# Optimization experiments

Measured on AMD Instinct MI355X. Metric: run time of the kernel, lower is better.

## Reference

```python
import jax, jax.numpy as jnp
import numpy as np

NS, BS, U, NR, NT, D = 256, 7, 8, 4, 8, 2
ITERS, HID = 3, 200
P, NOISE = 100.0, 1e-7
CIN = 2 * NT * D  # block input width: flattened Z1 and Z2


def setup_inputs() -> dict:
    key = jax.random.key(0)
    ks = jax.random.split(key, 21)
    rn = lambda k, s: jax.random.normal(k, s, dtype=jnp.float32)
    inp = {
        'H_re': rn(ks[0], (NS, BS, BS, U, NR, NT)),
        'H_im': rn(ks[1], (NS, BS, BS, U, NR, NT)),
        'V_re': rn(ks[2], (NS, BS, U, NT, D)),
        'V_im': rn(ks[3], (NS, BS, U, NT, D)),
        'w': jnp.ones((U,), jnp.float32),
        'W1_re': rn(ks[4], (ITERS, HID, CIN)) * 0.05,
        'W1_im': rn(ks[5], (ITERS, HID, CIN)) * 0.05,
        'b1_re': rn(ks[6], (ITERS, HID)) * 0.05,
        'b1_im': rn(ks[7], (ITERS, HID)) * 0.05,
        'W2_re': rn(ks[8], (ITERS, HID, HID)) * 0.05,
        'W2_im': rn(ks[9], (ITERS, HID, HID)) * 0.05,
        'b2_re': rn(ks[10], (ITERS, HID)) * 0.05,
        'b2_im': rn(ks[11], (ITERS, HID)) * 0.05,
        'W3_re': rn(ks[12], (ITERS, HID, HID)) * 0.05,
        'W3_im': rn(ks[13], (ITERS, HID, HID)) * 0.05,
        'b3_re': rn(ks[14], (ITERS, HID)) * 0.05,
        'b3_im': rn(ks[15], (ITERS, HID)) * 0.05,
        'W4_re': rn(ks[16], (ITERS, 1, HID)) * 0.05,
        'W4_im': rn(ks[17], (ITERS, 1, HID)) * 0.05,
        'b4_re': rn(ks[18], (ITERS, 1)) * 0.05,
        'b4_im': rn(ks[19], (ITERS, 1)) * 0.05,
    }
    return inp


def _crelu(x):
    # ComplexReLU: relu on real part, imaginary part passes through
    return jax.nn.relu(x.real) + 1j * x.imag


def _clin(x, W, b):
    # torch Linear with complex weights: x @ W.T + b
    return jnp.einsum('...i,oi->...o', x, W) + b


def _iteration(H, V, w, p):
    n = H.shape[0]
    Z = V
    # HV[n,k,l,i,j] = H[n,k,l,i] @ V[n,k,j]  -> [n,BS,BS,U,U,NR,D]
    HV = jnp.einsum('nklirt,nkjtd->nklijrd', H, V)
    ab = jnp.arange(BS)
    au = jnp.arange(U)
    HV2 = HV[:, ab, ab][:, :, au, au]  # HV[:,k,k,i,i] -> [n,BS,U,NR,D]
    # T[n,k,l,i,j] = HV @ HV^H -> [n,BS,BS,U,U,NR,NR]
    T = jnp.einsum('nklijrd,nklijsd->nklijrs', HV, HV.conj())
    I_r = jnp.eye(NR, dtype=HV.dtype)
    # U[n,l,u] = noise*I + sum_{k,j} T[n,k,l,u,j]
    Usum = NOISE * I_r + T.sum(axis=(1, 4))  # [n,BS,U,NR,NR]
    Y = jnp.linalg.solve(Usum, HV2)
    Td = T[:, ab, ab][:, :, au, au]  # T[:,l,l,u,u]
    F = Usum - Td
    Gamma = jnp.einsum('nlurd,nlure->nlude', HV2.conj(), jnp.linalg.solve(F, HV2))
    IG = jnp.eye(D, dtype=HV.dtype) + Gamma  # [n,BS,U,D,D]
    # A[n,l,m,u] = H[n,l,m,u].mH @ Y[n,m,u] -> [n,BS,BS,U,NT,D]
    A = jnp.einsum('nlmurt,nmurd->nlmutd', H.conj(), Y)
    # L[n,l,u] = sum_m A @ IG[m,u] @ A^H -> [n,BS,U,NT,NT]
    L = jnp.einsum('nlmutd,nmude,nlmuse->nluts', A, IG, A.conj())
    All = A[:, ab, ab]  # A[:,l,l] -> [n,BS,U,NT,D]
    Lam = jnp.einsum('nlutd,nlude->nlute', All, IG)
    wv = w.astype(HV.dtype)[None, None, :, None, None]
    Lam = Lam * wv
    L = L * wv
    Z2 = Lam - jnp.einsum('nluts,nlusd->nlutd', L, Z)
    inp = jnp.concatenate([Z.reshape(n, BS, U, NT * D), Z2.reshape(n, BS, U, NT * D)], -1)
    W1, b1, W2, b2, W3, b3, W4, b4 = p
    h = _crelu(_clin(inp, W1, b1))
    h = _crelu(_clin(h, W2, b2))
    h = _crelu(_clin(h, W3, b3))
    step = _clin(h, W4, b4).real  # [n,BS,U,1]
    Vn = Z + step[..., None] * Z2
    fro = (jnp.abs(Vn) ** 2).sum((-2, -1)).sum(2)  # [n,BS]
    scale = jnp.where(fro > P, jnp.sqrt(P / fro), 1.0)
    return Vn * scale[:, :, None, None, None].astype(Vn.dtype)


def reference(H_re, H_im, V_re, V_im, w, W1_re, W1_im, b1_re, b1_im, W2_re, W2_im, b2_re, b2_im, W3_re, W3_im, b3_re, b3_im, W4_re, W4_im, b4_re, b4_im):
    H = (H_re + 1j * H_im).astype(jnp.complex64)
    V = (V_re + 1j * V_im).astype(jnp.complex64)
    # init_input power normalization per (sample, BS)
    fro0 = (jnp.abs(V) ** 2).sum((-2, -1)).sum(2)
    V = V * jnp.sqrt(P / fro0)[:, :, None, None, None].astype(V.dtype)
    c64 = jnp.complex64
    Ws = [(W1_re + 1j * W1_im).astype(c64), (b1_re + 1j * b1_im).astype(c64),
          (W2_re + 1j * W2_im).astype(c64), (b2_re + 1j * b2_im).astype(c64),
          (W3_re + 1j * W3_im).astype(c64), (b3_re + 1j * b3_im).astype(c64),
          (W4_re + 1j * W4_im).astype(c64), (b4_re + 1j * b4_im).astype(c64)]
    for it in range(ITERS):
        p = tuple(a[it] for a in Ws)
        V = _iteration(H, V, w, p)
    return jnp.stack([V.real, V.imag], axis=-1)
```

## Files before the change

kernel.cpp:

```cpp
#include <hip/hip_runtime.h>
#include <math.h>

#define NS 256
#define BS 7
#define UU 8
#define NR 4
#define NT 8
#define DD 2
#define HID 200
#define CIN 32
#define PP 100.0f
#define NOISEF 1e-7f

typedef _Float16 f16x8 __attribute__((ext_vector_type(8)));
typedef float f32x4 __attribute__((ext_vector_type(4)));

#define AST 424
#define AST0 104
#define NTILES 28
#define B1_KC 3
#define B23_KC 13
#define B1_HALVES (B1_KC*NTILES*64*8)
#define B23_HALVES (B23_KC*NTILES*64*8)
#define BITER_HALVES (B1_HALVES + 2*B23_HALVES)

__device__ void chol_solve(const float2 (*A)[NR], const float2 (*B)[DD], float2 (*X)[DD]) {
  float2 L[NR][NR];
  for (int j = 0; j < NR; ++j) {
    float d = A[j][j].x;
    for (int k = 0; k < j; ++k) d -= L[j][k].x * L[j][k].x + L[j][k].y * L[j][k].y;
    float ld = sqrtf(fmaxf(d, 1e-30f));
    L[j][j] = make_float2(ld, 0.f);
    float inv = 1.f / ld;
    for (int i = j + 1; i < NR; ++i) {
      float sr = A[i][j].x, si = A[i][j].y;
      for (int k = 0; k < j; ++k) {
        float2 a = L[i][k], b = L[j][k];
        sr -= a.x * b.x + a.y * b.y;
        si -= a.y * b.x - a.x * b.y;
      }
      L[i][j] = make_float2(sr * inv, si * inv);
    }
  }
  for (int c = 0; c < DD; ++c) {
    float2 z[NR];
    for (int i = 0; i < NR; ++i) {
      float sr = B[i][c].x, si = B[i][c].y;
      for (int k = 0; k < i; ++k) {
        float2 a = L[i][k], zz = z[k];
        sr -= a.x * zz.x - a.y * zz.y;
        si -= a.x * zz.y + a.y * zz.x;
      }
      float inv = 1.f / L[i][i].x;
      z[i] = make_float2(sr * inv, si * inv);
    }
    for (int i = NR - 1; i >= 0; --i) {
      float sr = z[i].x, si = z[i].y;
      for (int k = i + 1; k < NR; ++k) {
        float2 a = L[k][i], xx = X[k][c];
        sr -= a.x * xx.x + a.y * xx.y;
        si -= a.x * xx.y - a.y * xx.x;
      }
      float inv = 1.f / L[i][i].x;
      X[i][c] = make_float2(sr * inv, si * inv);
    }
  }
}

__global__ void k_norm0(const float* __restrict__ Vre, const float* __restrict__ Vim,
                        float2* __restrict__ Vcur) {
  int nl = blockIdx.x;
  int tid = threadIdx.x;
  size_t base = (size_t)nl * 128;
  float re = Vre[base + tid], im = Vim[base + tid];
  float p = re * re + im * im;
  p += __shfl_down(p, 32); p += __shfl_down(p, 16); p += __shfl_down(p, 8);
  p += __shfl_down(p, 4);  p += __shfl_down(p, 2);  p += __shfl_down(p, 1);
  __shared__ float sred[2];
  if ((tid & 63) == 0) sred[tid >> 6] = p;
  __syncthreads();
  float fro = sred[0] + sred[1];
  float sc = sqrtf(PP / fro);
  Vcur[base + tid] = make_float2(re * sc, im * sc);
}

__global__ __launch_bounds__(512) void k_hv(const float* __restrict__ Hre,
    const float* __restrict__ Him, const float2* __restrict__ Vcur,
    float2* __restrict__ Yb, float2* __restrict__ IGb) {
  int nl = blockIdx.x; int l = nl % BS; int n = nl / BS;
  int tid = threadIdx.x;
  int wave = tid >> 6;
  int lane = tid & 63;
  int k = lane >> 3, j = lane & 7;

  __shared__ float2 Hs[1820];
  __shared__ float2 Vs[952];
  __shared__ float2 GsL[8][10];
  __shared__ float2 TdL[8][10];
  __shared__ float2 HV2L[8][8];

  for (int idx = tid; idx < 1792; idx += 512) {
    int kk = idx >> 8, irt = idx & 255;
    size_t off = ((size_t)(n * BS + kk) * BS + l) * 256 + irt;
    Hs[kk * 260 + irt] = make_float2(Hre[off], Him[off]);
  }
  const float2* Vn = Vcur + (size_t)n * 896;
  for (int idx = tid; idx < 896; idx += 512) {
    int kj = idx >> 4, td = idx & 15;
    Vs[kj * 17 + td] = Vn[idx];
  }
  __syncthreads();

  float2 Gu[10];
  #pragma unroll
  for (int q = 0; q < 10; ++q) Gu[q] = make_float2(0.f, 0.f);
  float2 hv[4][2];
  #pragma unroll
  for (int r = 0; r < 4; ++r)
    #pragma unroll
    for (int d = 0; d < 2; ++d) hv[r][d] = make_float2(0.f, 0.f);

  if (k < 7) {
    float2 v[8][2];
    const float2* vp = &Vs[(k * 8 + j) * 17];
    #pragma unroll
    for (int t = 0; t < 8; ++t) { v[t][0] = vp[2 * t]; v[t][1] = vp[2 * t + 1]; }
    #pragma unroll
    for (int r = 0; r < 4; ++r) {
      const float2* hp = &Hs[k * 260 + wave * 32 + r * 8];
      #pragma unroll
      for (int t = 0; t < 8; ++t) {
        float2 h = hp[t];
        #pragma unroll
        for (int d = 0; d < 2; ++d) {
          hv[r][d].x += h.x * v[t][d].x - h.y * v[t][d].y;
          hv[r][d].y += h.x * v[t][d].y + h.y * v[t][d].x;
        }
      }
    }
    int ui = 0;
    #pragma unroll
    for (int r = 0; r < 4; ++r)
      #pragma unroll
      for (int s = r; s < 4; ++s) {
        float gr = 0.f, gi = 0.f;
        #pragma unroll
        for (int d = 0; d < 2; ++d) {
          float2 a = hv[r][d], c = hv[s][d];
          gr += a.x * c.x + a.y * c.y;
          gi += a.y * c.x - a.x * c.y;
        }
        Gu[ui] = make_float2(gr, gi);
        ++ui;
      }
  }
  if (k == l && j == wave) {
    #pragma unroll
    for (int q = 0; q < 10; ++q) TdL[wave][q] = Gu[q];
    #pragma unroll
    for (int r = 0; r < 4; ++r)
      #pragma unroll
      for (int d = 0; d < 2; ++d)
        HV2L[wave][r * 2 + d] = hv[r][d];
  }
  #pragma unroll
  for (int m = 1; m < 64; m <<= 1) {
    #pragma unroll
    for (int q = 0; q < 10; ++q) {
      Gu[q].x += __shfl_xor(Gu[q].x, m);
      Gu[q].y += __shfl_xor(Gu[q].y, m);
    }
  }
  if (lane == 0) {
    #pragma unroll
    for (int q = 0; q < 10; ++q) GsL[wave][q] = Gu[q];
  }
  __syncthreads();

  if (tid < 16) {
    int i = tid & 7, which = tid >> 3;
    float2 M[NR][NR];
    int ui = 0;
    #pragma unroll
    for (int r = 0; r < 4; ++r)
      #pragma unroll
      for (int s = r; s < 4; ++s) {
        float2 g = GsL[i][ui];
        if (which) { float2 td = TdL[i][ui]; g.x -= td.x; g.y -= td.y; }
        ++ui;
        M[r][s] = g;
        M[s][r] = make_float2(g.x, -g.y);
      }
    #pragma unroll
    for (int r = 0; r < 4; ++r) { M[r][r].x += NOISEF; M[r][r].y = 0.f; }
    float2 Bv[NR][DD], X[NR][DD];
    #pragma unroll
    for (int x = 0; x < 8; ++x) Bv[x >> 1][x & 1] = HV2L[i][x];
    chol_solve(M, Bv, X);
    size_t b = (size_t)nl * 8 + i;
    if (!which) {
      #pragma unroll
      for (int x = 0; x < 8; ++x) Yb[b * 8 + x] = X[x >> 1][x & 1];
    } else {
      #pragma unroll
      for (int d = 0; d < DD; ++d)
        #pragma unroll
        for (int e = 0; e < DD; ++e) {
          float gr = (d == e) ? 1.f : 0.f, gi = 0.f;
          #pragma unroll
          for (int r = 0; r < NR; ++r) {
            float2 a = Bv[r][d], x = X[r][e];
            gr += a.x * x.x + a.y * x.y;
            gi += a.x * x.y - a.y * x.x;
          }
          IGb[b * 4 + d * 2 + e] = make_float2(gr, gi);
        }
    }
  }
}

__global__ __launch_bounds__(256) void k_stage2(const float* __restrict__ Hre,
    const float* __restrict__ Him, const float2* __restrict__ Vcur,
    const float2* __restrict__ Yb, const float2* __restrict__ IGb,
    const float* __restrict__ w, float2* __restrict__ Z2out) {
  int nl = blockIdx.x; int l = nl % BS; int n = nl / BS;
  int tid = threadIdx.x;
  __shared__ float2 SM[3686];
  float2* Hsm  = SM;
  float2* Bsm  = SM;
  float2* Lsm  = SM + 952;
  float2* Ysm  = SM + 1792;
  float2* IGsm = SM + 2247;
  float2* Asm  = SM + 2478;
  float2* Lamm = SM + 3430;
  float2* Zlm  = SM + 3558;

  size_t hbase = ((size_t)n * BS + l) * 1792;
  for (int idx = tid; idx < 1792; idx += 256) {
    int t = idx & 7, r = (idx >> 3) & 3, u = (idx >> 5) & 7, m = idx >> 8;
    Hsm[((u * 4 + r) * 7 + m) * 8 + t] = make_float2(Hre[hbase + idx], Him[hbase + idx]);
  }
  const float2* yp = Yb + (size_t)n * 448;
  for (int idx = tid; idx < 448; idx += 256)
    Ysm[(idx >> 6) * 65 + (idx & 63)] = yp[idx];
  const float2* igp = IGb + (size_t)n * 224;
  if (tid < 224) IGsm[(tid >> 5) * 33 + (tid & 31)] = igp[tid];
  const float2* zp = Vcur + (size_t)nl * 128;
  if (tid < 128) Zlm[tid] = zp[tid];
  __syncthreads();

  for (int idx = tid; idx < 896; idx += 256) {
    int u = idx / 112, rem = idx % 112, m = rem >> 4, t = (rem >> 1) & 7, d = rem & 1;
    float ar = 0.f, ai = 0.f;
    #pragma unroll
    for (int r = 0; r < NR; ++r) {
      float2 h = Hsm[((u * 4 + r) * 7 + m) * 8 + t];
      float2 y = Ysm[m * 65 + u * 8 + r * 2 + d];
      ar += h.x * y.x + h.y * y.y;
      ai += h.x * y.y - h.y * y.x;
    }
    Asm[u * 119 + m * 17 + t * 2 + d] = make_float2(ar, ai);
  }
  __syncthreads();

  for (int idx = tid; idx < 896; idx += 256) {
    int u = idx / 112, rem = idx % 112, m = rem >> 4, t = (rem >> 1) & 7, e = rem & 1;
    float br = 0.f, bi = 0.f;
    #pragma unroll
    for (int d = 0; d < DD; ++d) {
      float2 a = Asm[u * 119 + m * 17 + t * 2 + d];
      float2 g = IGsm[m * 33 + u * 4 + d * 2 + e];
      br += a.x * g.x - a.y * g.y;
      bi += a.x * g.y + a.y * g.x;
    }
    Bsm[u * 119 + m * 17 + t * 2 + e] = make_float2(br, bi);
  }
  __syncthreads();

  for (int idx = tid; idx < 512; idx += 256) {
    int u = idx >> 6, t = (idx >> 3) & 7, s = idx & 7;
    float lr = 0.f, li = 0.f;
    #pragma unroll
    for (int m = 0; m < BS; ++m)
      #pragma unroll
      for (int e = 0; e < DD; ++e) {
        float2 bb = Bsm[u * 119 + m * 17 + t * 2 + e];
        float2 ac = Asm[u * 119 + m * 17 + s * 2 + e];
        lr += bb.x * ac.x + bb.y * ac.y;
        li += bb.y * ac.x - bb.x * ac.y;
      }
    float wu = w[u];
    Lsm[(u * 8 + t) * 8 + s] = make_float2(lr * wu, li * wu);
  }
  if (tid < 128) {
    int u = tid >> 4, t = (tid >> 1) & 7, e = tid & 1;
    float ar = 0.f, ai = 0.f;
    #pragma unroll
    for (int d = 0; d < DD; ++d) {
      float2 a = Asm[u * 119 + l * 17 + t * 2 + d];
      float2 g = IGsm[l * 33 + u * 4 + d * 2 + e];
      ar += a.x * g.x - a.y * g.y;
      ai += a.x * g.y + a.y * g.x;
    }
    float wu = w[u];
    Lamm[u * 16 + t * 2 + e] = make_float2(ar * wu, ai * wu);
  }
  __syncthreads();

  if (tid < 128) {
    int u = tid >> 4, t = (tid >> 1) & 7, d = tid & 1;
    float2 lam = Lamm[u * 16 + t * 2 + d];
    float zr = lam.x, zi = lam.y;
    #pragma unroll
    for (int s = 0; s < NT; ++s) {
      float2 Lts = Lsm[(u * 8 + t) * 8 + s];
      float2 z = Zlm[u * 16 + s * 2 + d];
      zr -= Lts.x * z.x - Lts.y * z.y;
      zi -= Lts.x * z.y + Lts.y * z.x;
    }
    Z2out[(size_t)nl * 128 + u * 16 + t * 2 + d] = make_float2(zr, zi);
  }
}

__global__ __launch_bounds__(256) void k_pack(
    const float* __restrict__ W1re, const float* __restrict__ W1im,
    const float* __restrict__ b1re, const float* __restrict__ b1im,
    const float* __restrict__ W2re, const float* __restrict__ W2im,
    const float* __restrict__ b2re, const float* __restrict__ b2im,
    const float* __restrict__ W3re, const float* __restrict__ W3im,
    const float* __restrict__ b3re, const float* __restrict__ b3im,
    _Float16* __restrict__ Bout) {
  int gid = blockIdx.x * 256 + threadIdx.x;
  int lane = gid & 63;
  int rest = gid >> 6;
  int nt = rest % NTILES;
  int id2 = rest / NTILES;
  if (id2 >= 87) return;
  int iter = id2 / 29, kk = id2 % 29;
  int layer, kc;
  if (kk < 3)       { layer = 0; kc = kk; }
  else if (kk < 16) { layer = 1; kc = kk - 3; }
  else              { layer = 2; kc = kk - 16; }
  const float *Wr, *Wi, *br, *bi;
  if (layer == 0) { Wr = W1re + iter*HID*CIN; Wi = W1im + iter*HID*CIN; br = b1re + iter*HID; bi = b1im + iter*HID; }
  else if (layer == 1) { Wr = W2re + iter*HID*HID; Wi = W2im + iter*HID*HID; br = b2re + iter*HID; bi = b2im + iter*HID; }
  else { Wr = W3re + iter*HID*HID; Wi = W3im + iter*HID*HID; br = b3re + iter*HID; bi = b3im + iter*HID; }
  int c = nt * 16 + (lane & 15);
  int o = c >> 1; int odd = c & 1;
  f16x8 frag;
  #pragma unroll
  for (int j = 0; j < 8; ++j) {
    int k = kc * 32 + (lane >> 4) * 8 + j;
    float v = 0.f;
    if (o < HID) {
      if (layer == 0) {
        if (k < 32)       v = odd ? Wi[o*32 + k] : Wr[o*32 + k];
        else if (k < 64)  { int i = k - 32; v = odd ? Wr[o*32 + i] : -Wi[o*32 + i]; }
        else if (k == 64) v = odd ? bi[o] : br[o];
      } else {
        if (k < 200)       v = odd ? Wi[o*200 + k] : Wr[o*200 + k];
        else if (k == 207) v = odd ? bi[o] : br[o];
        else if (k >= 208 && k < 408) { int i = k - 208; v = odd ? Wr[o*200 + i] : -Wi[o*200 + i]; }
      }
    }
    frag[j] = (_Float16)v;
  }
  size_t off = (size_t)iter * BITER_HALVES
             + (layer == 0 ? 0 : (layer == 1 ? B1_HALVES : (B1_HALVES + B23_HALVES)))
             + ((size_t)(kc * NTILES + nt) * 64 + lane) * 8;
  *(f16x8*)(Bout + off) = frag;
}

template<int ASTRIDE, int KC>
__device__ inline void do_gemm(const _Float16* Ain,
                               const _Float16* __restrict__ Bg,
                               _Float16* Aout, int wr, int wc, int lane) {
  f32x4 acc[2][7];
  #pragma unroll
  for (int rt = 0; rt < 2; ++rt)
    #pragma unroll
    for (int nt = 0; nt < 7; ++nt)
      acc[rt][nt] = (f32x4){0.f, 0.f, 0.f, 0.f};
  const int r0 = (lane & 15) + wr * 32, g = lane >> 4;
  const _Float16* bp0 = Bg + ((size_t)(wc * 7) * 64 + lane) * 8;
  f16x8 b[7];
  #pragma unroll
  for (int nt = 0; nt < 7; ++nt) b[nt] = *(const f16x8*)(bp0 + nt * 512);
  f16x8 a0 = *(const f16x8*)(Ain + r0 * ASTRIDE + 8 * g);
  f16x8 a1 = *(const f16x8*)(Ain + (r0 + 16) * ASTRIDE + 8 * g);
  #pragma unroll
  for (int kc = 0; kc < KC; ++kc) {
    f16x8 a0n, a1n, bn[7];
    if (kc + 1 < KC) {
      const _Float16* bpn = bp0 + (size_t)(kc + 1) * (NTILES * 512);
      #pragma unroll
      for (int nt = 0; nt < 7; ++nt) bn[nt] = *(const f16x8*)(bpn + nt * 512);
      a0n = *(const f16x8*)(Ain + r0 * ASTRIDE + (kc + 1) * 32 + 8 * g);
      a1n = *(const f16x8*)(Ain + (r0 + 16) * ASTRIDE + (kc + 1) * 32 + 8 * g);
    }
    #pragma unroll
    for (int nt = 0; nt < 7; ++nt) {
      acc[0][nt] = __builtin_amdgcn_mfma_f32_16x16x32_f16(a0, b[nt], acc[0][nt], 0, 0, 0);
      acc[1][nt] = __builtin_amdgcn_mfma_f32_16x16x32_f16(a1, b[nt], acc[1][nt], 0, 0, 0);
    }
    if (kc + 1 < KC) {
      a0 = a0n; a1 = a1n;
      #pragma unroll
      for (int nt = 0; nt < 7; ++nt) b[nt] = bn[nt];
    }
  }
  int cbase = wc * 7 * 16 + (lane & 15);
  #pragma unroll
  for (int nt = 0; nt < 7; ++nt) {
    int c = cbase + nt * 16;
    int o = c >> 1;
    bool isre = !(c & 1);
    if (o < HID) {
      _Float16* outp = Aout + (isre ? o : 208 + o);
      #pragma unroll
      for (int rt = 0; rt < 2; ++rt)
        #pragma unroll
        for (int q = 0; q < 4; ++q) {
          float v = acc[rt][nt][q];
          if (isre) v = fmaxf(v, 0.f);
          outp[(size_t)(wr * 32 + rt * 16 + g * 4 + q) * AST] = (_Float16)v;
        }
    }
  }
}

__global__ __launch_bounds__(512, 2) void k_mlp_mfma(
    const float2* __restrict__ Vcur, const float2* __restrict__ Z2,
    const _Float16* __restrict__ Bp,
    const float* __restrict__ W4re, const float* __restrict__ W4im,
    const float* __restrict__ b4re,
    float2* __restrict__ Vout) {
  int b = blockIdx.x;
  int tid = threadIdx.x;
  int wave = tid >> 6, lane = tid & 63;
  int wr = wave >> 2, wc = wave & 3;

  __shared__ _Float16 A0[64 * AST0];
  __shared__ _Float16 Abuf[2][64 * AST];
  __shared__ float2 Zs[64][16];
  __shared__ float2 Z2s[64][16];
  __shared__ float w4s[2][HID];
  __shared__ float stepv[64];
  __shared__ float scs[8];

  for (int idx = tid; idx < 1024; idx += 512) {
    ((float2*)Zs)[idx]  = Vcur[(size_t)b * 1024 + idx];
    ((float2*)Z2s)[idx] = Z2[(size_t)b * 1024 + idx];
  }
  for (int idx = tid; idx < HID; idx += 512) {
    w4s[0][idx] = W4re[idx];
    w4s[1][idx] = W4im[idx];
  }
  __syncthreads();

  for (int idx = tid; idx < 64 * AST0; idx += 512) {
    int m = idx / AST0, c = idx % AST0;
    float v;
    if (c < 64) {
      int f = c & 31;
      float2 z = (f < 16) ? Zs[m][f] : Z2s[m][f - 16];
      v = (c >= 32) ? z.y : z.x;
    } else v = (c == 64) ? 1.f : 0.f;
    A0[m * AST0 + c] = (_Float16)v;
  }
  for (int idx = tid; idx < 2 * 64 * 16; idx += 512) {
    int buf = idx >> 10, rem = idx & 1023, m = rem >> 4, p = rem & 15;
    int c = (p < 8) ? (200 + p) : (400 + p);
    Abuf[buf][m * AST + c] = (p == 7) ? (_Float16)1.f : (_Float16)0.f;
  }
  __syncthreads();

  do_gemm<AST0, B1_KC>(A0, Bp, &Abuf[0][0], wr, wc, lane);
  __syncthreads();
  do_gemm<AST, B23_KC>(&Abuf[0][0], Bp + B1_HALVES, &Abuf[1][0], wr, wc, lane);
  __syncthreads();
  do_gemm<AST, B23_KC>(&Abuf[1][0], Bp + B1_HALVES + B23_HALVES, &Abuf[0][0], wr, wc, lane);
  __syncthreads();

  {
    int m = tid >> 3, q = tid & 7;
    float acc = 0.f;
    for (int o = q; o < HID; o += 8) {
      float hr = (float)Abuf[0][m * AST + o];
      float hi = (float)Abuf[0][m * AST + 208 + o];
      acc += hr * w4s[0][o] - hi * w4s[1][o];
    }
    acc += __shfl_down(acc, 4, 8);
    acc += __shfl_down(acc, 2, 8);
    acc += __shfl_down(acc, 1, 8);
    if (q == 0) stepv[m] = acc + b4re[0];
  }
  __syncthreads();

  for (int idx = tid; idx < 1024; idx += 512) {
    int m = idx >> 4, f = idx & 15;
    float st = stepv[m];
    float2 z = Zs[m][f], z2 = Z2s[m][f];
    Zs[m][f] = make_float2(fmaf(st, z2.x, z.x), fmaf(st, z2.y, z.y));
  }
  __syncthreads();

  {
    const float2* vp = &Zs[wave * 8][0];
    float2 v0 = vp[lane * 2], v1 = vp[lane * 2 + 1];
    float p = v0.x * v0.x + v0.y * v0.y + v1.x * v1.x + v1.y * v1.y;
    p += __shfl_down(p, 32); p += __shfl_down(p, 16); p += __shfl_down(p, 8);
    p += __shfl_down(p, 4);  p += __shfl_down(p, 2);  p += __shfl_down(p, 1);
    if (lane == 0) scs[wave] = (p > PP) ? sqrtf(PP / p) : 1.f;
  }
  __syncthreads();
  for (int idx = tid; idx < 1024; idx += 512) {
    float sc = scs[idx >> 7];
    float2 v = ((float2*)Zs)[idx];
    Vout[(size_t)b * 1024 + idx] = make_float2(v.x * sc, v.y * sc);
  }
}

extern "C" void kernel_launch(void* const* d_in, const int* in_sizes, int n_in,
                              void* d_out, int out_size, void* d_ws, size_t ws_size,
                              hipStream_t stream) {
  const float* Hre  = (const float*)d_in[0];
  const float* Him  = (const float*)d_in[1];
  const float* Vre  = (const float*)d_in[2];
  const float* Vim  = (const float*)d_in[3];
  const float* w    = (const float*)d_in[4];
  const float* W1re = (const float*)d_in[5];
  const float* W1im = (const float*)d_in[6];
  const float* b1re = (const float*)d_in[7];
  const float* b1im = (const float*)d_in[8];
  const float* W2re = (const float*)d_in[9];
  const float* W2im = (const float*)d_in[10];
  const float* b2re = (const float*)d_in[11];
  const float* b2im = (const float*)d_in[12];
  const float* W3re = (const float*)d_in[13];
  const float* W3im = (const float*)d_in[14];
  const float* b3re = (const float*)d_in[15];
  const float* b3im = (const float*)d_in[16];
  const float* W4re = (const float*)d_in[17];
  const float* W4im = (const float*)d_in[18];
  const float* b4re = (const float*)d_in[19];

  const size_t NV = (size_t)NS * BS * UU * NT * DD;
  const size_t NB = (size_t)NS * BS * UU;
  float2* Vcur = (float2*)d_ws;
  float2* Z2b  = Vcur + NV;
  float2* Yb   = Z2b + NV;
  float2* IGb  = Yb + NB * 8;
  _Float16* Bpack = (_Float16*)(IGb + NB * 4);

  k_pack<<<609, 256, 0, stream>>>(W1re, W1im, b1re, b1im, W2re, W2im, b2re, b2im,
                                  W3re, W3im, b3re, b3im, Bpack);
  k_norm0<<<NS * BS, 128, 0, stream>>>(Vre, Vim, Vcur);
  for (int it = 0; it < 3; ++it) {
    k_hv<<<NS * BS, 512, 0, stream>>>(Hre, Him, Vcur, Yb, IGb);
    k_stage2<<<NS * BS, 256, 0, stream>>>(Hre, Him, Vcur, Yb, IGb, w, Z2b);
    float2* vout = (it == 2) ? (float2*)d_out : Vcur;
    k_mlp_mfma<<<NS * BS / 8, 512, 0, stream>>>(Vcur, Z2b,
        Bpack + (size_t)it * BITER_HALVES,
        W4re + it * HID, W4im + it * HID, b4re + it, vout);
  }
}
```

Measured before the change: 258.6 us.

## Move per-block Cholesky solves out of k_hv into a separate parallel kernel

Before, each 512-thread k_hv block ended with a barrier and then only 16 threads ran serial Cholesky solves while the rest of the block sat idle. Now k_hv writes the reduced Gram matrices, diagonal terms and HV2 vectors to global buffers and exits. A new k_solve kernel runs all 28672 solves with one thread each across 112 blocks. The cost is an extra launch per iteration plus a global write and read round trip for the intermediates, which need more workspace.

```diff
diff --git a/kernel.cpp b/kernel.cpp
--- a/kernel.cpp
+++ b/kernel.cpp
@@ -86,7 +86,7 @@
 
 __global__ __launch_bounds__(512) void k_hv(const float* __restrict__ Hre,
     const float* __restrict__ Him, const float2* __restrict__ Vcur,
-    float2* __restrict__ Yb, float2* __restrict__ IGb) {
+    float2* __restrict__ Gsb, float2* __restrict__ Tdb, float2* __restrict__ HV2b) {
   int nl = blockIdx.x; int l = nl % BS; int n = nl / BS;
   int tid = threadIdx.x;
   int wave = tid >> 6;
@@ -95,9 +95,6 @@
 
   __shared__ float2 Hs[1820];
   __shared__ float2 Vs[952];
-  __shared__ float2 GsL[8][10];
-  __shared__ float2 TdL[8][10];
-  __shared__ float2 HV2L[8][8];
 
   for (int idx = tid; idx < 1792; idx += 512) {
     int kk = idx >> 8, irt = idx & 255;
@@ -155,13 +152,12 @@
       }
   }
   if (k == l && j == wave) {
-    #pragma unroll
-    for (int q = 0; q < 10; ++q) TdL[wave][q] = Gu[q];
-    #pragma unroll
-    for (int r = 0; r < 4; ++r)
-      #pragma unroll
-      for (int d = 0; d < 2; ++d)
-        HV2L[wave][r * 2 + d] = hv[r][d];
+    float2* tdp = Tdb + (size_t)(nl * 8 + wave) * 10;
+    #pragma unroll
+    for (int q = 0; q < 10; ++q) tdp[q] = Gu[q];
+    float2* h2p = HV2b + (size_t)(nl * 8 + wave) * 8;
+    #pragma unroll
+    for (int x = 0; x < 8; ++x) h2p[x] = hv[x >> 1][x & 1];
   }
   #pragma unroll
   for (int m = 1; m < 64; m <<= 1) {
@@ -172,50 +168,64 @@
     }
   }
   if (lane == 0) {
-    #pragma unroll
-    for (int q = 0; q < 10; ++q) GsL[wave][q] = Gu[q];
-  }
-  __syncthreads();
-
-  if (tid < 16) {
-    int i = tid & 7, which = tid >> 3;
-    float2 M[NR][NR];
+    float2* gp = Gsb + (size_t)(nl * 8 + wave) * 10;
+    #pragma unroll
+    for (int q = 0; q < 10; ++q) gp[q] = Gu[q];
+  }
+}
+
+__global__ __launch_bounds__(256) void k_solve(const float2* __restrict__ Gsb,
+    const float2* __restrict__ Tdb, const float2* __restrict__ HV2b,
+    float2* __restrict__ Yb, float2* __restrict__ IGb) {
+  int gid = blockIdx.x * 256 + threadIdx.x;
+  int which = (gid >= 14336) ? 1 : 0;
+  int b = gid - which * 14336;
+
+  float2 G[10];
+  const float2* gp = Gsb + (size_t)b * 10;
+  #pragma unroll
+  for (int q = 0; q < 10; ++q) G[q] = gp[q];
+  if (which) {
+    const float2* tp = Tdb + (size_t)b * 10;
+    #pragma unroll
+    for (int q = 0; q < 10; ++q) { float2 t = tp[q]; G[q].x -= t.x; G[q].y -= t.y; }
+  }
+  float2 M[NR][NR];
+  {
     int ui = 0;
     #pragma unroll
     for (int r = 0; r < 4; ++r)
       #pragma unroll
       for (int s = r; s < 4; ++s) {
-        float2 g = GsL[i][ui];
-        if (which) { float2 td = TdL[i][ui]; g.x -= td.x; g.y -= td.y; }
+        M[r][s] = G[ui];
+        M[s][r] = make_float2(G[ui].x, -G[ui].y);
         ++ui;
-        M[r][s] = g;
-        M[s][r] = make_float2(g.x, -g.y);
       }
     #pragma unroll
     for (int r = 0; r < 4; ++r) { M[r][r].x += NOISEF; M[r][r].y = 0.f; }
-    float2 Bv[NR][DD], X[NR][DD];
-    #pragma unroll
-    for (int x = 0; x < 8; ++x) Bv[x >> 1][x & 1] = HV2L[i][x];
-    chol_solve(M, Bv, X);
-    size_t b = (size_t)nl * 8 + i;
-    if (!which) {
-      #pragma unroll
-      for (int x = 0; x < 8; ++x) Yb[b * 8 + x] = X[x >> 1][x & 1];
-    } else {
-      #pragma unroll
-      for (int d = 0; d < DD; ++d)
+  }
+  float2 Bv[NR][DD], X[NR][DD];
+  const float2* hp = HV2b + (size_t)b * 8;
+  #pragma unroll
+  for (int x = 0; x < 8; ++x) Bv[x >> 1][x & 1] = hp[x];
+  chol_solve(M, Bv, X);
+  if (!which) {
+    #pragma unroll
+    for (int x = 0; x < 8; ++x) Yb[(size_t)b * 8 + x] = X[x >> 1][x & 1];
+  } else {
+    #pragma unroll
+    for (int d = 0; d < DD; ++d)
+      #pragma unroll
+      for (int e = 0; e < DD; ++e) {
+        float gr = (d == e) ? 1.f : 0.f, gi = 0.f;
         #pragma unroll
-        for (int e = 0; e < DD; ++e) {
-          float gr = (d == e) ? 1.f : 0.f, gi = 0.f;
-          #pragma unroll
-          for (int r = 0; r < NR; ++r) {
-            float2 a = Bv[r][d], x = X[r][e];
-            gr += a.x * x.x + a.y * x.y;
-            gi += a.x * x.y - a.y * x.x;
-          }
-          IGb[b * 4 + d * 2 + e] = make_float2(gr, gi);
+        for (int r = 0; r < NR; ++r) {
+          float2 a = Bv[r][d], x = X[r][e];
+          gr += a.x * x.x + a.y * x.y;
+          gi += a.x * x.y - a.y * x.x;
         }
-    }
+        IGb[(size_t)b * 4 + d * 2 + e] = make_float2(gr, gi);
+      }
   }
 }
 
@@ -551,13 +561,17 @@
   float2* Z2b  = Vcur + NV;
   float2* Yb   = Z2b + NV;
   float2* IGb  = Yb + NB * 8;
-  _Float16* Bpack = (_Float16*)(IGb + NB * 4);
+  float2* Gsb  = IGb + NB * 4;
+  float2* Tdb  = Gsb + NB * 10;
+  float2* HV2b = Tdb + NB * 10;
+  _Float16* Bpack = (_Float16*)(HV2b + NB * 8);
 
   k_pack<<<609, 256, 0, stream>>>(W1re, W1im, b1re, b1im, W2re, W2im, b2re, b2im,
                                   W3re, W3im, b3re, b3im, Bpack);
   k_norm0<<<NS * BS, 128, 0, stream>>>(Vre, Vim, Vcur);
   for (int it = 0; it < 3; ++it) {
-    k_hv<<<NS * BS, 512, 0, stream>>>(Hre, Him, Vcur, Yb, IGb);
+    k_hv<<<NS * BS, 512, 0, stream>>>(Hre, Him, Vcur, Gsb, Tdb, HV2b);
+    k_solve<<<112, 256, 0, stream>>>(Gsb, Tdb, HV2b, Yb, IGb);
     k_stage2<<<NS * BS, 256, 0, stream>>>(Hre, Him, Vcur, Yb, IGb, w, Z2b);
     float2* vout = (it == 2) ? (float2*)d_out : Vcur;
     k_mlp_mfma<<<NS * BS / 8, 512, 0, stream>>>(Vcur, Z2b,
```

Result: faster. 252.1 us (-2.5%).

## Process all BS columns per sample in one k_hv block with double-buffered H loads

Applied to the files above, without the earlier changes.

The HV/Gram kernel now launches one block per sample instead of one per (sample, l). Each block loops over the 7 l values and prefetches the next H slice into registers while computing the current one in a double-buffered LDS tile. V is loaded once per sample rather than once per l, and global loads use float4. The Cholesky solves are batched at the end across 112 threads. The cost is far fewer blocks (256 on a GPU with many CUs) and a serialized l loop, so parallelism and latency hiding may suffer.

```diff
diff --git a/kernel.cpp b/kernel.cpp
--- a/kernel.cpp
+++ b/kernel.cpp
@@ -84,137 +84,166 @@
   Vcur[base + tid] = make_float2(re * sc, im * sc);
 }
 
-__global__ __launch_bounds__(512) void k_hv(const float* __restrict__ Hre,
+__global__ __launch_bounds__(512, 2) void k_hv_n(const float* __restrict__ Hre,
     const float* __restrict__ Him, const float2* __restrict__ Vcur,
     float2* __restrict__ Yb, float2* __restrict__ IGb) {
-  int nl = blockIdx.x; int l = nl % BS; int n = nl / BS;
+  int n = blockIdx.x;
   int tid = threadIdx.x;
   int wave = tid >> 6;
   int lane = tid & 63;
-  int k = lane >> 3, j = lane & 7;
-
-  __shared__ float2 Hs[1820];
+  int kl = lane >> 3, j = lane & 7;
+
+  __shared__ float2 Hbuf[2][1820];
   __shared__ float2 Vs[952];
-  __shared__ float2 GsL[8][10];
-  __shared__ float2 TdL[8][10];
-  __shared__ float2 HV2L[8][8];
-
-  for (int idx = tid; idx < 1792; idx += 512) {
-    int kk = idx >> 8, irt = idx & 255;
-    size_t off = ((size_t)(n * BS + kk) * BS + l) * 256 + irt;
-    Hs[kk * 260 + irt] = make_float2(Hre[off], Him[off]);
-  }
+  __shared__ float2 GsL[56][10];
+  __shared__ float2 TdL[56][10];
+  __shared__ float2 HV2L[56][8];
+
+  const int kk = tid >> 6;
+  const int irt = (tid & 63) * 4;
+
   const float2* Vn = Vcur + (size_t)n * 896;
-  for (int idx = tid; idx < 896; idx += 512) {
-    int kj = idx >> 4, td = idx & 15;
-    Vs[kj * 17 + td] = Vn[idx];
-  }
-  __syncthreads();
-
-  float2 Gu[10];
-  #pragma unroll
-  for (int q = 0; q < 10; ++q) Gu[q] = make_float2(0.f, 0.f);
-  float2 hv[4][2];
-  #pragma unroll
-  for (int r = 0; r < 4; ++r)
-    #pragma unroll
-    for (int d = 0; d < 2; ++d) hv[r][d] = make_float2(0.f, 0.f);
-
-  if (k < 7) {
-    float2 v[8][2];
-    const float2* vp = &Vs[(k * 8 + j) * 17];
+  if (tid < 448) {
+    size_t off = ((size_t)(n * BS + kk) * BS + 0) * 256 + irt;
+    float4 r0 = *(const float4*)(Hre + off);
+    float4 i0 = *(const float4*)(Him + off);
+    float2* hb = &Hbuf[0][kk * 260 + irt];
+    ((float4*)hb)[0] = make_float4(r0.x, i0.x, r0.y, i0.y);
+    ((float4*)hb)[1] = make_float4(r0.z, i0.z, r0.w, i0.w);
+    int row = tid >> 3, c = (tid & 7) * 2;
+    float4 vv = *(const float4*)((const float*)(Vn + row * 16 + c));
+    Vs[row * 17 + c]     = make_float2(vv.x, vv.y);
+    Vs[row * 17 + c + 1] = make_float2(vv.z, vv.w);
+  }
+  __syncthreads();
+
+  float2 v[8][2];
+  if (kl < 7) {
+    const float2* vp = &Vs[(kl * 8 + j) * 17];
     #pragma unroll
     for (int t = 0; t < 8; ++t) { v[t][0] = vp[2 * t]; v[t][1] = vp[2 * t + 1]; }
-    #pragma unroll
-    for (int r = 0; r < 4; ++r) {
-      const float2* hp = &Hs[k * 260 + wave * 32 + r * 8];
-      #pragma unroll
-      for (int t = 0; t < 8; ++t) {
-        float2 h = hp[t];
+  }
+
+  float4 hreN, himN;
+  #pragma unroll 1
+  for (int l = 0; l < BS; ++l) {
+    if (l + 1 < BS && tid < 448) {
+      size_t off = ((size_t)(n * BS + kk) * BS + (l + 1)) * 256 + irt;
+      hreN = *(const float4*)(Hre + off);
+      himN = *(const float4*)(Him + off);
+    }
+    const float2* Hc = &Hbuf[l & 1][0];
+
+    float2 Gu[10];
+    #pragma unroll
+    for (int q = 0; q < 10; ++q) Gu[q] = make_float2(0.f, 0.f);
+    float2 hv[4][2];
+    #pragma unroll
+    for (int r = 0; r < 4; ++r)
+      #pragma unroll
+      for (int d = 0; d < 2; ++d) hv[r][d] = make_float2(0.f, 0.f);
+
+    if (kl < 7) {
+      #pragma unroll
+      for (int r = 0; r < 4; ++r) {
+        const float2* hp = &Hc[kl * 260 + wave * 32 + r * 8];
         #pragma unroll
-        for (int d = 0; d < 2; ++d) {
-          hv[r][d].x += h.x * v[t][d].x - h.y * v[t][d].y;
-          hv[r][d].y += h.x * v[t][d].y + h.y * v[t][d].x;
+        for (int t = 0; t < 8; ++t) {
+          float2 h = hp[t];
+          #pragma unroll
+          for (int d = 0; d < 2; ++d) {
+            hv[r][d].x += h.x * v[t][d].x - h.y * v[t][d].y;
+            hv[r][d].y += h.x * v[t][d].y + h.y * v[t][d].x;
+          }
         }
       }
-    }
-    int ui = 0;
-    #pragma unroll
-    for (int r = 0; r < 4; ++r)
-      #pragma unroll
-      for (int s = r; s < 4; ++s) {
-        float gr = 0.f, gi = 0.f;
+      int ui = 0;
+      #pragma unroll
+      for (int r = 0; r < 4; ++r)
         #pragma unroll
-        for (int d = 0; d < 2; ++d) {
-          float2 a = hv[r][d], c = hv[s][d];
-          gr += a.x * c.x + a.y * c.y;
-          gi += a.y * c.x - a.x * c.y;
+        for (int s = r; s < 4; ++s) {
+          float gr = 0.f, gi = 0.f;
+          #pragma unroll
+          for (int d = 0; d < 2; ++d) {
+            float2 a = hv[r][d], c = hv[s][d];
+            gr += a.x * c.x + a.y * c.y;
+            gi += a.y * c.x - a.x * c.y;
+          }
+          Gu[ui] = make_float2(gr, gi);
+          ++ui;
         }
-        Gu[ui] = make_float2(gr, gi);
-        ++ui;
-      }
-  }
-  if (k == l && j == wave) {
-    #pragma unroll
-    for (int q = 0; q < 10; ++q) TdL[wave][q] = Gu[q];
-    #pragma unroll
-    for (int r = 0; r < 4; ++r)
-      #pragma unroll
-      for (int d = 0; d < 2; ++d)
-        HV2L[wave][r * 2 + d] = hv[r][d];
-  }
-  #pragma unroll
-  for (int m = 1; m < 64; m <<= 1) {
-    #pragma unroll
-    for (int q = 0; q < 10; ++q) {
-      Gu[q].x += __shfl_xor(Gu[q].x, m);
-      Gu[q].y += __shfl_xor(Gu[q].y, m);
-    }
-  }
-  if (lane == 0) {
-    #pragma unroll
-    for (int q = 0; q < 10; ++q) GsL[wave][q] = Gu[q];
-  }
-  __syncthreads();
-
-  if (tid < 16) {
-    int i = tid & 7, which = tid >> 3;
-    float2 M[NR][NR];
-    int ui = 0;
-    #pragma unroll
-    for (int r = 0; r < 4; ++r)
-      #pragma unroll
-      for (int s = r; s < 4; ++s) {
-        float2 g = GsL[i][ui];
-        if (which) { float2 td = TdL[i][ui]; g.x -= td.x; g.y -= td.y; }
-        ++ui;
-        M[r][s] = g;
-        M[s][r] = make_float2(g.x, -g.y);
-      }
-    #pragma unroll
-    for (int r = 0; r < 4; ++r) { M[r][r].x += NOISEF; M[r][r].y = 0.f; }
-    float2 Bv[NR][DD], X[NR][DD];
-    #pragma unroll
-    for (int x = 0; x < 8; ++x) Bv[x >> 1][x & 1] = HV2L[i][x];
-    chol_solve(M, Bv, X);
-    size_t b = (size_t)nl * 8 + i;
-    if (!which) {
-      #pragma unroll
-      for (int x = 0; x < 8; ++x) Yb[b * 8 + x] = X[x >> 1][x & 1];
-    } else {
-      #pragma unroll
-      for (int d = 0; d < DD; ++d)
+    }
+    if (kl == l && j == wave) {
+      #pragma unroll
+      for (int q = 0; q < 10; ++q) TdL[l * 8 + wave][q] = Gu[q];
+      #pragma unroll
+      for (int x = 0; x < 8; ++x) HV2L[l * 8 + wave][x] = hv[x >> 1][x & 1];
+    }
+    #pragma unroll
+    for (int m = 1; m < 64; m <<= 1) {
+      #pragma unroll
+      for (int q = 0; q < 10; ++q) {
+        Gu[q].x += __shfl_xor(Gu[q].x, m);
+        Gu[q].y += __shfl_xor(Gu[q].y, m);
+      }
+    }
+    if (lane == 0) {
+      #pragma unroll
+      for (int q = 0; q < 10; ++q) GsL[l * 8 + wave][q] = Gu[q];
+    }
+
+    __syncthreads();
+    if (l + 1 < BS) {
+      if (tid < 448) {
+        float2* hb = &Hbuf[(l + 1) & 1][kk * 260 + irt];
+        ((float4*)hb)[0] = make_float4(hreN.x, himN.x, hreN.y, himN.y);
+        ((float4*)hb)[1] = make_float4(hreN.z, himN.z, hreN.w, himN.w);
+      }
+      __syncthreads();
+    }
+  }
+
+  if (tid < 128) {
+    int which = tid >> 6;
+    int b = tid - which * 64;
+    if (b < 56) {
+      float2 M[NR][NR];
+      int ui = 0;
+      #pragma unroll
+      for (int r = 0; r < 4; ++r)
         #pragma unroll
-        for (int e = 0; e < DD; ++e) {
-          float gr = (d == e) ? 1.f : 0.f, gi = 0.f;
+        for (int s = r; s < 4; ++s) {
+          float2 g = GsL[b][ui];
+          if (which) { float2 td = TdL[b][ui]; g.x -= td.x; g.y -= td.y; }
+          ++ui;
+          M[r][s] = g;
+          M[s][r] = make_float2(g.x, -g.y);
+        }
+      #pragma unroll
+      for (int r = 0; r < 4; ++r) { M[r][r].x += NOISEF; M[r][r].y = 0.f; }
+      float2 Bv[NR][DD], X[NR][DD];
+      #pragma unroll
+      for (int x = 0; x < 8; ++x) Bv[x >> 1][x & 1] = HV2L[b][x];
+      chol_solve(M, Bv, X);
+      size_t gb = (size_t)n * 56 + b;
+      if (!which) {
+        #pragma unroll
+        for (int x = 0; x < 8; ++x) Yb[gb * 8 + x] = X[x >> 1][x & 1];
+      } else {
+        #pragma unroll
+        for (int d = 0; d < DD; ++d)
           #pragma unroll
-          for (int r = 0; r < NR; ++r) {
-            float2 a = Bv[r][d], x = X[r][e];
-            gr += a.x * x.x + a.y * x.y;
-            gi += a.x * x.y - a.y * x.x;
+          for (int e = 0; e < DD; ++e) {
+            float gr = (d == e) ? 1.f : 0.f, gi = 0.f;
+            #pragma unroll
+            for (int r = 0; r < NR; ++r) {
+              float2 a = Bv[r][d], x = X[r][e];
+              gr += a.x * x.x + a.y * x.y;
+              gi += a.x * x.y - a.y * x.x;
+            }
+            IGb[gb * 4 + d * 2 + e] = make_float2(gr, gi);
           }
-          IGb[b * 4 + d * 2 + e] = make_float2(gr, gi);
-        }
+      }
     }
   }
 }
@@ -557,7 +586,7 @@
                                   W3re, W3im, b3re, b3im, Bpack);
   k_norm0<<<NS * BS, 128, 0, stream>>>(Vre, Vim, Vcur);
   for (int it = 0; it < 3; ++it) {
-    k_hv<<<NS * BS, 512, 0, stream>>>(Hre, Him, Vcur, Yb, IGb);
+    k_hv_n<<<NS, 512, 0, stream>>>(Hre, Him, Vcur, Yb, IGb);
     k_stage2<<<NS * BS, 256, 0, stream>>>(Hre, Him, Vcur, Yb, IGb, w, Z2b);
     float2* vout = (it == 2) ? (float2*)d_out : Vcur;
     k_mlp_mfma<<<NS * BS / 8, 512, 0, stream>>>(Vcur, Z2b,
```

Result: no change. 262.6 us (+1.5%).

## Restructure k_hv to one wave per block with register accumulation over k

Applied to the files above, without the earlier changes.

Rewrites k_hv so each block is a single 64-thread wave where lane = (user i, stream j), looping over the 7 transmitting BSs and accumulating the Gram terms in registers instead of staging H and V in shared memory across 8 waves. Cross-lane reduction shrinks to 8 lanes, and the diagonal term and HV2 are gathered with shuffles, so shared memory and block barriers go away. Loads of H and V now go straight from global memory as float4. The trade-off is much less parallelism per block, with a serial k loop per lane and more redundant global reads of H and V.

```diff
diff --git a/kernel.cpp b/kernel.cpp
--- a/kernel.cpp
+++ b/kernel.cpp
@@ -84,60 +84,53 @@
   Vcur[base + tid] = make_float2(re * sc, im * sc);
 }
 
-__global__ __launch_bounds__(512) void k_hv(const float* __restrict__ Hre,
+__global__ __launch_bounds__(64) void k_hv(const float* __restrict__ Hre,
     const float* __restrict__ Him, const float2* __restrict__ Vcur,
     float2* __restrict__ Yb, float2* __restrict__ IGb) {
-  int nl = blockIdx.x; int l = nl % BS; int n = nl / BS;
-  int tid = threadIdx.x;
-  int wave = tid >> 6;
-  int lane = tid & 63;
-  int k = lane >> 3, j = lane & 7;
-
-  __shared__ float2 Hs[1820];
-  __shared__ float2 Vs[952];
-  __shared__ float2 GsL[8][10];
-  __shared__ float2 TdL[8][10];
-  __shared__ float2 HV2L[8][8];
-
-  for (int idx = tid; idx < 1792; idx += 512) {
-    int kk = idx >> 8, irt = idx & 255;
-    size_t off = ((size_t)(n * BS + kk) * BS + l) * 256 + irt;
-    Hs[kk * 260 + irt] = make_float2(Hre[off], Him[off]);
-  }
-  const float2* Vn = Vcur + (size_t)n * 896;
-  for (int idx = tid; idx < 896; idx += 512) {
-    int kj = idx >> 4, td = idx & 15;
-    Vs[kj * 17 + td] = Vn[idx];
-  }
-  __syncthreads();
-
-  float2 Gu[10];
-  #pragma unroll
-  for (int q = 0; q < 10; ++q) Gu[q] = make_float2(0.f, 0.f);
-  float2 hv[4][2];
-  #pragma unroll
-  for (int r = 0; r < 4; ++r)
-    #pragma unroll
-    for (int d = 0; d < 2; ++d) hv[r][d] = make_float2(0.f, 0.f);
-
-  if (k < 7) {
+  int b = blockIdx.x; int l = b % BS, n = b / BS;
+  int lane = threadIdx.x;
+  int i = lane >> 3, j = lane & 7;
+
+  float2 G[10], td[10], hv2[8];
+  #pragma unroll
+  for (int q = 0; q < 10; ++q) { G[q] = make_float2(0.f, 0.f); td[q] = make_float2(0.f, 0.f); }
+  #pragma unroll
+  for (int x = 0; x < 8; ++x) hv2[x] = make_float2(0.f, 0.f);
+
+  #pragma unroll
+  for (int k = 0; k < BS; ++k) {
+    size_t hoff = ((size_t)n * 49 + k * 7 + l) * 256 + i * 32;
+    const float* hr = Hre + hoff;
+    const float* hi = Him + hoff;
+    const float2* vp = Vcur + ((size_t)n * 56 + k * 8 + j) * 16;
     float2 v[8][2];
-    const float2* vp = &Vs[(k * 8 + j) * 17];
-    #pragma unroll
-    for (int t = 0; t < 8; ++t) { v[t][0] = vp[2 * t]; v[t][1] = vp[2 * t + 1]; }
+    #pragma unroll
+    for (int q = 0; q < 8; ++q) {
+      float4 vv = *(const float4*)(vp + 2 * q);
+      v[q][0] = make_float2(vv.x, vv.y);
+      v[q][1] = make_float2(vv.z, vv.w);
+    }
+    float2 hv[4][2];
     #pragma unroll
     for (int r = 0; r < 4; ++r) {
-      const float2* hp = &Hs[k * 260 + wave * 32 + r * 8];
+      float4 a0 = *(const float4*)(hr + r * 8);
+      float4 a1 = *(const float4*)(hr + r * 8 + 4);
+      float4 b0 = *(const float4*)(hi + r * 8);
+      float4 b1 = *(const float4*)(hi + r * 8 + 4);
+      float hx[8] = {a0.x, a0.y, a0.z, a0.w, a1.x, a1.y, a1.z, a1.w};
+      float hy[8] = {b0.x, b0.y, b0.z, b0.w, b1.x, b1.y, b1.z, b1.w};
+      float2 ac0 = make_float2(0.f, 0.f), ac1 = make_float2(0.f, 0.f);
       #pragma unroll
       for (int t = 0; t < 8; ++t) {
-        float2 h = hp[t];
-        #pragma unroll
-        for (int d = 0; d < 2; ++d) {
-          hv[r][d].x += h.x * v[t][d].x - h.y * v[t][d].y;
-          hv[r][d].y += h.x * v[t][d].y + h.y * v[t][d].x;
-        }
-      }
-    }
+        float rx = hx[t], ry = hy[t];
+        ac0.x += rx * v[t][0].x - ry * v[t][0].y;
+        ac0.y += rx * v[t][0].y + ry * v[t][0].x;
+        ac1.x += rx * v[t][1].x - ry * v[t][1].y;
+        ac1.y += rx * v[t][1].y + ry * v[t][1].x;
+      }
+      hv[r][0] = ac0; hv[r][1] = ac1;
+    }
+    bool diag = (k == l) && (j == i);
     int ui = 0;
     #pragma unroll
     for (int r = 0; r < 4; ++r)
@@ -150,57 +143,60 @@
           gr += a.x * c.x + a.y * c.y;
           gi += a.y * c.x - a.x * c.y;
         }
-        Gu[ui] = make_float2(gr, gi);
+        G[ui].x += gr; G[ui].y += gi;
+        if (diag) td[ui] = make_float2(gr, gi);
         ++ui;
       }
-  }
-  if (k == l && j == wave) {
-    #pragma unroll
-    for (int q = 0; q < 10; ++q) TdL[wave][q] = Gu[q];
-    #pragma unroll
-    for (int r = 0; r < 4; ++r)
-      #pragma unroll
-      for (int d = 0; d < 2; ++d)
-        HV2L[wave][r * 2 + d] = hv[r][d];
-  }
-  #pragma unroll
-  for (int m = 1; m < 64; m <<= 1) {
+    if (diag) {
+      #pragma unroll
+      for (int x = 0; x < 8; ++x) hv2[x] = hv[x >> 1][x & 1];
+    }
+  }
+
+  #pragma unroll
+  for (int m = 1; m < 8; m <<= 1) {
     #pragma unroll
     for (int q = 0; q < 10; ++q) {
-      Gu[q].x += __shfl_xor(Gu[q].x, m);
-      Gu[q].y += __shfl_xor(Gu[q].y, m);
-    }
-  }
-  if (lane == 0) {
-    #pragma unroll
-    for (int q = 0; q < 10; ++q) GsL[wave][q] = Gu[q];
-  }
-  __syncthreads();
-
-  if (tid < 16) {
-    int i = tid & 7, which = tid >> 3;
+      G[q].x += __shfl_xor(G[q].x, m);
+      G[q].y += __shfl_xor(G[q].y, m);
+    }
+  }
+  int src = i * 9;
+  float2 tdr[10], h2r[8];
+  #pragma unroll
+  for (int q = 0; q < 10; ++q) {
+    tdr[q].x = __shfl(td[q].x, src);
+    tdr[q].y = __shfl(td[q].y, src);
+  }
+  #pragma unroll
+  for (int x = 0; x < 8; ++x) {
+    h2r[x].x = __shfl(hv2[x].x, src);
+    h2r[x].y = __shfl(hv2[x].y, src);
+  }
+
+  if (j < 2) {
     float2 M[NR][NR];
     int ui = 0;
     #pragma unroll
     for (int r = 0; r < 4; ++r)
       #pragma unroll
       for (int s = r; s < 4; ++s) {
-        float2 g = GsL[i][ui];
-        if (which) { float2 td = TdL[i][ui]; g.x -= td.x; g.y -= td.y; }
-        ++ui;
+        float2 g = G[ui];
+        if (j == 1) { g.x -= tdr[ui].x; g.y -= tdr[ui].y; }
         M[r][s] = g;
         M[s][r] = make_float2(g.x, -g.y);
+        ++ui;
       }
     #pragma unroll
     for (int r = 0; r < 4; ++r) { M[r][r].x += NOISEF; M[r][r].y = 0.f; }
     float2 Bv[NR][DD], X[NR][DD];
     #pragma unroll
-    for (int x = 0; x < 8; ++x) Bv[x >> 1][x & 1] = HV2L[i][x];
+    for (int x = 0; x < 8; ++x) Bv[x >> 1][x & 1] = h2r[x];
     chol_solve(M, Bv, X);
-    size_t b = (size_t)nl * 8 + i;
-    if (!which) {
-      #pragma unroll
-      for (int x = 0; x < 8; ++x) Yb[b * 8 + x] = X[x >> 1][x & 1];
+    size_t gb = (size_t)n * 56 + l * 8 + i;
+    if (j == 0) {
+      #pragma unroll
+      for (int x = 0; x < 8; ++x) Yb[gb * 8 + x] = X[x >> 1][x & 1];
     } else {
       #pragma unroll
       for (int d = 0; d < DD; ++d)
@@ -213,7 +209,7 @@
             gr += a.x * x.x + a.y * x.y;
             gi += a.x * x.y - a.y * x.x;
           }
-          IGb[b * 4 + d * 2 + e] = make_float2(gr, gi);
+          IGb[gb * 4 + d * 2 + e] = make_float2(gr, gi);
         }
     }
   }
@@ -557,7 +553,7 @@
                                   W3re, W3im, b3re, b3im, Bpack);
   k_norm0<<<NS * BS, 128, 0, stream>>>(Vre, Vim, Vcur);
   for (int it = 0; it < 3; ++it) {
-    k_hv<<<NS * BS, 512, 0, stream>>>(Hre, Him, Vcur, Yb, IGb);
+    k_hv<<<NS * BS, 64, 0, stream>>>(Hre, Him, Vcur, Yb, IGb);
     k_stage2<<<NS * BS, 256, 0, stream>>>(Hre, Him, Vcur, Yb, IGb, w, Z2b);
     float2* vout = (it == 2) ? (float2*)d_out : Vcur;
     k_mlp_mfma<<<NS * BS / 8, 512, 0, stream>>>(Vcur, Z2b,
```

After: 244.2 us. -5.6%, faster.
